# Performance work log

Hardware: AMD Instinct MI355X
Metric: run time of the kernel (lower is better)

Reference implementation:

```python
import jax, jax.numpy as jnp
import numpy as np
import math

ANSWER_LEN = 11; D_MODEL = 6; FFN_DIM = 3; HEAD_DIM = 3; MAX_SEQ_LEN = 34
N_HEADS = 2; POS_DIM = 3; TOK_DIM = 3; VOCAB_SIZE = 14; MAX_DIGITS = 10
EOS_TOKEN = 12; EQUALS_TOKEN = 11; PAD_TOKEN = 13; PLUS_TOKEN = 10
B, T = 65536, 34


def _spiral(i, period):
    return (math.cos(2 * math.pi * i / period), math.sin(2 * math.pi * i / period), i / max(period - 1, 1))


def _build_pos_enc():
    N_POS = 10
    pe = np.zeros((MAX_SEQ_LEN, POS_DIM), dtype=np.float32)
    for i in range(MAX_DIGITS):
        pe[i] = _spiral(i, N_POS)
    for i in range(MAX_DIGITS):
        pe[11 + i] = _spiral(i, N_POS)
    for i in range(min(ANSWER_LEN, N_POS)):
        pe[22 + i] = _spiral(i, N_POS)
    pe[32] = [0.0, 0.0, 1.5]
    pe[10] = [2.0, 0.0, -1.0]
    pe[21] = [0.0, 2.0, -1.0]
    pe[33] = [-2.0, 0.0, -1.0]
    return pe


def _build_tok_emb():
    emb = np.zeros((VOCAB_SIZE, TOK_DIM), dtype=np.float32)
    for d in range(10):
        emb[d] = _spiral(d, 10)
    emb[PLUS_TOKEN] = [2.0, 0.0, -1.0]
    emb[EQUALS_TOKEN] = [0.0, 2.0, -1.0]
    emb[EOS_TOKEN] = [-2.0, 0.0, -1.0]
    emb[PAD_TOKEN] = [0.0, -2.0, -1.0]
    return emb


def setup_inputs() -> dict:
    key = jax.random.key(0)
    ks = jax.random.split(key, 12)
    H = N_HEADS * HEAD_DIM  # 6

    def lin(k, out_d, in_d):
        bound = 1.0 / math.sqrt(in_d)
        return jax.random.uniform(k, (out_d, in_d), jnp.float32, -bound, bound)

    return {
        'idx': jax.random.randint(ks[0], (B, T), 0, VOCAB_SIZE),
        'tok_emb': jnp.asarray(_build_tok_emb()),
        'pos_enc': jnp.asarray(_build_pos_enc()),
        'q_w': lin(ks[1], H, POS_DIM),
        'k_w': lin(ks[2], H, POS_DIM),
        'v_w': lin(ks[3], H, TOK_DIM),
        'out_w': lin(ks[4], D_MODEL, H),
        'ln1_g': jnp.ones((D_MODEL,)), 'ln1_b': jnp.zeros((D_MODEL,)),
        'ln2_g': jnp.ones((D_MODEL,)), 'ln2_b': jnp.zeros((D_MODEL,)),
        'lnf_g': jnp.ones((D_MODEL,)), 'lnf_b': jnp.zeros((D_MODEL,)),
        'ffn_w1': lin(ks[5], FFN_DIM, D_MODEL),
        'ffn_b1': jax.random.uniform(ks[6], (FFN_DIM,), jnp.float32, -1/math.sqrt(D_MODEL), 1/math.sqrt(D_MODEL)),
        'ffn_w2': lin(ks[7], D_MODEL, FFN_DIM),
        'ffn_b2': jax.random.uniform(ks[8], (D_MODEL,), jnp.float32, -1/math.sqrt(FFN_DIM), 1/math.sqrt(FFN_DIM)),
        'head_w': lin(ks[9], TOK_DIM, D_MODEL),
    }


def _ln(x, g, b, eps=1e-5):
    mu = jnp.mean(x, -1, keepdims=True)
    var = jnp.mean((x - mu) ** 2, -1, keepdims=True)
    return (x - mu) * jax.lax.rsqrt(var + eps) * g + b


def reference(idx, tok_emb, pos_enc, q_w, k_w, v_w, out_w,
              ln1_g, ln1_b, ln2_g, ln2_b, lnf_g, lnf_b,
              ffn_w1, ffn_b1, ffn_w2, ffn_b2, head_w):
    b, t = idx.shape
    tok = tok_emb[idx]                              # [B,T,3]
    pos = jnp.broadcast_to(pos_enc[:t][None], (b, t, POS_DIM))
    x = jnp.concatenate([tok, pos], -1)             # [B,T,6]
    h = _ln(x, ln1_g, ln1_b)
    x_tok, x_pos = h[..., :TOK_DIM], h[..., TOK_DIM:]
    q = (x_pos @ q_w.T).reshape(b, t, N_HEADS, HEAD_DIM)
    k = (x_pos @ k_w.T).reshape(b, t, N_HEADS, HEAD_DIM)
    v = (x_tok @ v_w.T).reshape(b, t, N_HEADS, HEAD_DIM)
    attn = jnp.einsum('bqhd,bkhd->bhqk', q, k) / math.sqrt(HEAD_DIM)
    mask = jnp.tril(jnp.ones((t, t), dtype=bool))
    attn = jnp.where(mask[None, None], attn, -jnp.inf)
    attn = jax.nn.softmax(attn, -1)
    out = jnp.einsum('bhqk,bkhd->bqhd', attn, v).reshape(b, t, N_HEADS * HEAD_DIM)
    x = x + out @ out_w.T
    h2 = _ln(x, ln2_g, ln2_b)
    ffn = jax.nn.gelu(h2 @ ffn_w1.T + ffn_b1, approximate=False) @ ffn_w2.T + ffn_b2
    x = x + ffn
    x = _ln(x, lnf_g, lnf_b)
    return (x @ head_w.T) @ tok_emb.T               # [B,T,VOCAB]
```

## Files before the change

### kernel.cpp

```cpp
#include <hip/hip_runtime.h>
#include <math.h>

#define TT  34
#define VV  14
#define BLK 256

#if __has_builtin(__builtin_amdgcn_exp2f)
#define EXP2F(x) __builtin_amdgcn_exp2f(x)
#else
#define EXP2F(x) exp2f(x)
#endif


__global__ __launch_bounds__(BLK) void addtx_fwd(
    const int*   __restrict__ idx,
    const float* __restrict__ tok_emb,
    const float* __restrict__ pos_enc,
    const float* __restrict__ q_w,
    const float* __restrict__ k_w,
    const float* __restrict__ v_w,
    const float* __restrict__ out_w,
    const float* __restrict__ ln1_g, const float* __restrict__ ln1_b,
    const float* __restrict__ ln2_g, const float* __restrict__ ln2_b,
    const float* __restrict__ lnf_g, const float* __restrict__ lnf_b,
    const float* __restrict__ ffn_w1, const float* __restrict__ ffn_b1,
    const float* __restrict__ ffn_w2, const float* __restrict__ ffn_b2,
    const float* __restrict__ head_w,
    float* __restrict__ out)
{
    __shared__ float4 kvs[TT * VV * 3];
    __shared__ float  wsm[336];
    __shared__ int    idsb[308];

    const int tid = threadIdx.x;
    const int blk = blockIdx.x;

    {
        const int i = tid;
        if (i < 36)       wsm[i] = out_w[i];
        else if (i < 42)  wsm[i] = ln2_g[i - 36];
        else if (i < 48)  wsm[i] = ln2_b[i - 42];
        else if (i < 66)  wsm[i] = ffn_w1[i - 48];
        else if (i < 69)  wsm[i] = ffn_b1[i - 66];
        else if (i < 87)  wsm[i] = ffn_w2[i - 69];
        else if (i < 93)  wsm[i] = ffn_b2[i - 87];
        else if (i < 99)  wsm[i] = lnf_g[i - 93];
        else if (i < 105) wsm[i] = lnf_b[i - 99];
        else if (i < 189) {
            const int j = i - 105, v = j / 6, d = j - v * 6;
            wsm[i] = head_w[0 * 6 + d] * tok_emb[v * 3 + 0]
                   + head_w[1 * 6 + d] * tok_emb[v * 3 + 1]
                   + head_w[2 * 6 + d] * tok_emb[v * 3 + 2];
        }
        if (tid < 144) {
            const int k2 = 192 + tid;
            wsm[k2] = (k2 < 234) ? tok_emb[k2 - 192] : pos_enc[k2 - 234];
        }
    }

    const int ntot = (int)gridDim.x * BLK;
    const int b0   = (blk * BLK) / TT;
    {
        const int gb = b0 * TT;
        for (int e = tid; e < 308; e += BLK) {
            const int g = gb + e;
            idsb[e] = (g < ntot) ? idx[g] : 0;
        }
    }

    const float rs3l = 0.57735026918962576f * 1.4426950408889634f;
    for (int e = tid; e < TT * VV; e += BLK) {
        const int pos = e / VV, id = e - pos * VV;
        float x[6];
        x[0] = tok_emb[id * 3 + 0]; x[1] = tok_emb[id * 3 + 1]; x[2] = tok_emb[id * 3 + 2];
        x[3] = pos_enc[pos * 3 + 0]; x[4] = pos_enc[pos * 3 + 1]; x[5] = pos_enc[pos * 3 + 2];
        float mu = (x[0] + x[1] + x[2] + x[3] + x[4] + x[5]) * (1.0f / 6.0f);
        float var = 0.0f;
        #pragma unroll
        for (int d = 0; d < 6; ++d) { float dd = x[d] - mu; var += dd * dd; }
        const float rstd = rsqrtf(var * (1.0f / 6.0f) + 1e-5f);
        float h[6];
        #pragma unroll
        for (int d = 0; d < 6; ++d) h[d] = (x[d] - mu) * rstd * ln1_g[d] + ln1_b[d];
        float kk[6], vvv[6];
        #pragma unroll
        for (int r = 0; r < 6; ++r) {
            kk[r]  = (h[3] * k_w[r * 3 + 0] + h[4] * k_w[r * 3 + 1] + h[5] * k_w[r * 3 + 2]) * rs3l;
            vvv[r] =  h[0] * v_w[r * 3 + 0] + h[1] * v_w[r * 3 + 1] + h[2] * v_w[r * 3 + 2];
        }
        kvs[e * 3 + 0] = make_float4(kk[0], kk[1], kk[2], kk[3]);
        kvs[e * 3 + 1] = make_float4(kk[4], kk[5], vvv[0], vvv[1]);
        kvs[e * 3 + 2] = make_float4(vvv[2], vvv[3], vvv[4], vvv[5]);
    }
    __syncthreads();

    const int srank = (tid + ((blk & 3) << 6)) & (BLK - 1);
    const int r0 = (blk * BLK) % TT;
    const int m  = (TT - r0) % TT;
    int dsel, ksel;
    if (m < 18) {
        const int nA = (18 - m) << 3;
        if (srank < nA)            { dsel = m + (srank >> 3); ksel = srank & 7; }
        else if (srank < nA + 112) { const int r = srank - nA;       dsel = 18 + r / 7; ksel = r % 7; }
        else                       { const int r = srank - nA - 112; dsel = r >> 3;     ksel = r & 7; }
    } else {
        const int nA = (TT - m) * 7;
        if (srank < nA)            { dsel = m + srank / 7; ksel = srank % 7; }
        else if (srank < nA + 144) { const int r = srank - nA;       dsel = r >> 3;     ksel = r & 7; }
        else                       { const int r = srank - nA - 144; dsel = 18 + r / 7; ksel = r % 7; }
    }
    const int il   = dsel + ksel * TT;
    const int flat = blk * BLK + il;
    const int b    = flat / TT;
    const int t    = flat - b * TT;
    const int* __restrict__ rowL = idsb + (b - b0) * TT;

    float x[6];
    {
        const int mid = rowL[t];
        x[0] = wsm[192 + mid * 3]; x[1] = wsm[193 + mid * 3]; x[2] = wsm[194 + mid * 3];
        x[3] = wsm[234 + t * 3];   x[4] = wsm[235 + t * 3];   x[5] = wsm[236 + t * 3];
    }
    float q[6];
    {
        float mu = (x[0] + x[1] + x[2] + x[3] + x[4] + x[5]) * (1.0f / 6.0f);
        float var = 0.0f;
        #pragma unroll
        for (int d = 0; d < 6; ++d) { float dd = x[d] - mu; var += dd * dd; }
        const float rstd = rsqrtf(var * (1.0f / 6.0f) + 1e-5f);
        float h[6];
        #pragma unroll
        for (int d = 0; d < 6; ++d) h[d] = (x[d] - mu) * rstd * ln1_g[d] + ln1_b[d];
        #pragma unroll
        for (int r = 0; r < 6; ++r)
            q[r] = h[3] * q_w[r * 3 + 0] + h[4] * q_w[r * 3 + 1] + h[5] * q_w[r * 3 + 2];
    }

    float l0 = 0.f, l1 = 0.f;
    float a0 = 0.f, a1 = 0.f, a2 = 0.f, a3 = 0.f, a4 = 0.f, a5 = 0.f;
    int ids = rowL[0];
    int sb = 0;
    for (int s = 0; s <= t; ++s) {
        const float4* e4 = kvs + (sb + ids * 3);
        const float4 ka = e4[0];
        const float4 kb = e4[1];
        const float4 vb = e4[2];
        ids = rowL[s + 1];
        const float sc0 = q[0] * ka.x + q[1] * ka.y + q[2] * ka.z;
        const float sc1 = q[3] * ka.w + q[4] * kb.x + q[5] * kb.y;
        const float p0 = EXP2F(sc0);
        const float p1 = EXP2F(sc1);
        l0 += p0; l1 += p1;
        a0 += p0 * kb.z; a1 += p0 * kb.w; a2 += p0 * vb.x;
        a3 += p1 * vb.y; a4 += p1 * vb.z; a5 += p1 * vb.w;
        sb += VV * 3;
    }
    const float i0 = 1.0f / l0, i1 = 1.0f / l1;
    const float o6[6] = { a0 * i0, a1 * i0, a2 * i0, a3 * i1, a4 * i1, a5 * i1 };

    #pragma unroll
    for (int d = 0; d < 6; ++d) {
        float s = x[d];
        #pragma unroll
        for (int j = 0; j < 6; ++j) s += o6[j] * wsm[d * 6 + j];
        x[d] = s;
    }

    {
        float mu = (x[0] + x[1] + x[2] + x[3] + x[4] + x[5]) * (1.0f / 6.0f);
        float var = 0.0f;
        #pragma unroll
        for (int d = 0; d < 6; ++d) { float dd = x[d] - mu; var += dd * dd; }
        const float rstd = rsqrtf(var * (1.0f / 6.0f) + 1e-5f);
        float h2[6];
        #pragma unroll
        for (int d = 0; d < 6; ++d) h2[d] = (x[d] - mu) * rstd * wsm[36 + d] + wsm[42 + d];
        float g3[3];
        #pragma unroll
        for (int i = 0; i < 3; ++i) {
            float f = wsm[66 + i];
            #pragma unroll
            for (int d = 0; d < 6; ++d) f += h2[d] * wsm[48 + i * 6 + d];
            g3[i] = 0.5f * f * (1.0f + erff(f * 0.70710678118654752f));
        }
        #pragma unroll
        for (int d = 0; d < 6; ++d) {
            float s = x[d] + wsm[87 + d];
            #pragma unroll
            for (int i = 0; i < 3; ++i) s += g3[i] * wsm[69 + d * 3 + i];
            x[d] = s;
        }
    }

    float lg[VV];
    {
        float mu = (x[0] + x[1] + x[2] + x[3] + x[4] + x[5]) * (1.0f / 6.0f);
        float var = 0.0f;
        #pragma unroll
        for (int d = 0; d < 6; ++d) { float dd = x[d] - mu; var += dd * dd; }
        const float rstd = rsqrtf(var * (1.0f / 6.0f) + 1e-5f);
        float xf[6];
        #pragma unroll
        for (int d = 0; d < 6; ++d) xf[d] = (x[d] - mu) * rstd * wsm[93 + d] + wsm[99 + d];
        #pragma unroll
        for (int v = 0; v < VV; ++v) {
            float s = 0.0f;
            #pragma unroll
            for (int d = 0; d < 6; ++d) s += xf[d] * wsm[105 + v * 6 + d];
            lg[v] = s;
        }
    }

    __syncthreads();
    float2* lg2 = reinterpret_cast<float2*>(kvs);
    #pragma unroll
    for (int j = 0; j < 7; ++j)
        lg2[il * 7 + j] = make_float2(lg[2 * j], lg[2 * j + 1]);
    __syncthreads();
    const float2* s2 = reinterpret_cast<const float2*>(kvs);
    float2* __restrict__ ob2 = reinterpret_cast<float2*>(out + (size_t)blk * (BLK * VV));
    #pragma unroll
    for (int j = 0; j < 7; ++j)
        ob2[j * BLK + tid] = s2[j * BLK + tid];
}

extern "C" void kernel_launch(void* const* d_in, const int* in_sizes, int n_in,
                              void* d_out, int out_size, void* d_ws, size_t ws_size,
                              hipStream_t stream) {
    const int*   idx     = (const int*)  d_in[0];
    const float* tok_emb = (const float*)d_in[1];
    const float* pos_enc = (const float*)d_in[2];
    const float* q_w     = (const float*)d_in[3];
    const float* k_w     = (const float*)d_in[4];
    const float* v_w     = (const float*)d_in[5];
    const float* out_w   = (const float*)d_in[6];
    const float* ln1_g   = (const float*)d_in[7];
    const float* ln1_b   = (const float*)d_in[8];
    const float* ln2_g   = (const float*)d_in[9];
    const float* ln2_b   = (const float*)d_in[10];
    const float* lnf_g   = (const float*)d_in[11];
    const float* lnf_b   = (const float*)d_in[12];
    const float* ffn_w1  = (const float*)d_in[13];
    const float* ffn_b1  = (const float*)d_in[14];
    const float* ffn_w2  = (const float*)d_in[15];
    const float* ffn_b2  = (const float*)d_in[16];
    const float* head_w  = (const float*)d_in[17];
    float* out = (float*)d_out;

    const int n = in_sizes[0];
    const int blocks = n / BLK;
    addtx_fwd<<<blocks, BLK, 0, stream>>>(idx, tok_emb, pos_enc, q_w, k_w, v_w, out_w,
                                          ln1_g, ln1_b, ln2_g, ln2_b, lnf_g, lnf_b,
                                          ffn_w1, ffn_b1, ffn_w2, ffn_b2, head_w, out);
}
```

Measured before the change: 222.8 us.

## Remap blocks to 64-sequence by 4-position tiles with wave-uniform positions

Each block now handles 64 sequences and a chunk of up to 4 time positions, one wavefront per position. Every lane in a wave therefore runs the same attention loop length, which removes the divergence of the old mixed-position mapping. Block indices are swizzled so the 8 XCDs each take contiguous batch ranges. The idx tile is stored as bytes in a transposed layout, the K/V table is built only for the rows the block needs, and the final layernorm is folded into the head projection. In exchange, each block re-reads the same idx rows across 9 time chunks, and the output writes become strided with partial-row scatter.

```diff
diff --git a/kernel.cpp b/kernel.cpp
--- a/kernel.cpp
+++ b/kernel.cpp
@@ -4,6 +4,9 @@
 #define TT  34
 #define VV  14
 #define BLK 256
+#define BCH 64
+#define NCH 9
+#define IDP 68
 
 #if __has_builtin(__builtin_amdgcn_exp2f)
 #define EXP2F(x) __builtin_amdgcn_exp2f(x)
@@ -29,47 +32,59 @@
     float* __restrict__ out)
 {
     __shared__ float4 kvs[TT * VV * 3];
-    __shared__ float  wsm[336];
-    __shared__ int    idsb[308];
+    __shared__ float  wsm[176];
+    __shared__ unsigned char idsb[35 * IDP];
 
     const int tid = threadIdx.x;
-    const int blk = blockIdx.x;
-
-    {
+
+    const int bx   = blockIdx.x;
+    const int xcd  = bx & 7;
+    const int jj   = bx >> 3;
+    const int jd9  = jj / NCH;
+    const int tc   = jj - jd9 * NCH;
+    const int nbc8 = (int)gridDim.x / (NCH * 8);
+    const int bc   = xcd * nbc8 + jd9;
+    const int b0   = bc * BCH;
+    const int t_base = tc << 2;
+    const int nt   = (tc == 8) ? 2 : 4;
+    const int nst  = t_base + nt + ((tc == 8) ? 0 : 0);
+    const int nrow = (tc == 8) ? TT : (t_base + 4);
+
+    if (tid < 176) {
+        float val = 0.0f;
         const int i = tid;
-        if (i < 36)       wsm[i] = out_w[i];
-        else if (i < 42)  wsm[i] = ln2_g[i - 36];
-        else if (i < 48)  wsm[i] = ln2_b[i - 42];
-        else if (i < 66)  wsm[i] = ffn_w1[i - 48];
-        else if (i < 69)  wsm[i] = ffn_b1[i - 66];
-        else if (i < 87)  wsm[i] = ffn_w2[i - 69];
-        else if (i < 93)  wsm[i] = ffn_b2[i - 87];
-        else if (i < 99)  wsm[i] = lnf_g[i - 93];
-        else if (i < 105) wsm[i] = lnf_b[i - 99];
-        else if (i < 189) {
-            const int j = i - 105, v = j / 6, d = j - v * 6;
-            wsm[i] = head_w[0 * 6 + d] * tok_emb[v * 3 + 0]
-                   + head_w[1 * 6 + d] * tok_emb[v * 3 + 1]
-                   + head_w[2 * 6 + d] * tok_emb[v * 3 + 2];
-        }
-        if (tid < 144) {
-            const int k2 = 192 + tid;
-            wsm[k2] = (k2 < 234) ? tok_emb[k2 - 192] : pos_enc[k2 - 234];
-        }
-    }
-
-    const int ntot = (int)gridDim.x * BLK;
-    const int b0   = (blk * BLK) / TT;
+        if (i < 36)       val = out_w[i];
+        else if (i < 42)  val = ln2_g[i - 36];
+        else if (i < 48)  val = ln2_b[i - 42];
+        else if (i < 66)  val = ffn_w1[i - 48];
+        else if (i < 69)  val = ffn_b1[i - 66];
+        else if (i < 87)  val = ffn_w2[i - 69];
+        else if (i < 93)  val = ffn_b2[i - 87];
+        else if (i < 111) { const int k = i - 93, c = k / 6, d = k - c * 6;
+                            val = lnf_g[d] * head_w[c * 6 + d]; }
+        else if (i < 114) { const int c = i - 111; float s = 0.0f;
+                            #pragma unroll
+                            for (int d = 0; d < 6; ++d) s += lnf_g[d] * head_w[c * 6 + d];
+                            val = s; }
+        else if (i < 117) { const int c = i - 114; float s = 0.0f;
+                            #pragma unroll
+                            for (int d = 0; d < 6; ++d) s += lnf_b[d] * head_w[c * 6 + d];
+                            val = s; }
+        else if (i >= 120 && i < 162) val = tok_emb[i - 120];
+        wsm[i] = val;
+    }
+
     {
         const int gb = b0 * TT;
-        for (int e = tid; e < 308; e += BLK) {
-            const int g = gb + e;
-            idsb[e] = (g < ntot) ? idx[g] : 0;
-        }
+        for (int e = tid; e < BCH * TT; e += BLK) {
+            const int bl = e / TT, s = e - bl * TT;
+            idsb[s * IDP + bl] = (unsigned char)idx[gb + e];
+        }
+        if (tid < BCH) idsb[TT * IDP + tid] = 0;
     }
 
     const float rs3l = 0.57735026918962576f * 1.4426950408889634f;
-    for (int e = tid; e < TT * VV; e += BLK) {
+    for (int e = tid; e < nrow * VV; e += BLK) {
         const int pos = e / VV, id = e - pos * VV;
         float x[6];
         x[0] = tok_emb[id * 3 + 0]; x[1] = tok_emb[id * 3 + 1]; x[2] = tok_emb[id * 3 + 2];
@@ -94,134 +109,129 @@
     }
     __syncthreads();
 
-    const int srank = (tid + ((blk & 3) << 6)) & (BLK - 1);
-    const int r0 = (blk * BLK) % TT;
-    const int m  = (TT - r0) % TT;
-    int dsel, ksel;
-    if (m < 18) {
-        const int nA = (18 - m) << 3;
-        if (srank < nA)            { dsel = m + (srank >> 3); ksel = srank & 7; }
-        else if (srank < nA + 112) { const int r = srank - nA;       dsel = 18 + r / 7; ksel = r % 7; }
-        else                       { const int r = srank - nA - 112; dsel = r >> 3;     ksel = r & 7; }
-    } else {
-        const int nA = (TT - m) * 7;
-        if (srank < nA)            { dsel = m + srank / 7; ksel = srank % 7; }
-        else if (srank < nA + 144) { const int r = srank - nA;       dsel = r >> 3;     ksel = r & 7; }
-        else                       { const int r = srank - nA - 144; dsel = 18 + r / 7; ksel = r % 7; }
-    }
-    const int il   = dsel + ksel * TT;
-    const int flat = blk * BLK + il;
-    const int b    = flat / TT;
-    const int t    = flat - b * TT;
-    const int* __restrict__ rowL = idsb + (b - b0) * TT;
-
-    float x[6];
-    {
-        const int mid = rowL[t];
-        x[0] = wsm[192 + mid * 3]; x[1] = wsm[193 + mid * 3]; x[2] = wsm[194 + mid * 3];
-        x[3] = wsm[234 + t * 3];   x[4] = wsm[235 + t * 3];   x[5] = wsm[236 + t * 3];
-    }
-    float q[6];
-    {
-        float mu = (x[0] + x[1] + x[2] + x[3] + x[4] + x[5]) * (1.0f / 6.0f);
-        float var = 0.0f;
-        #pragma unroll
-        for (int d = 0; d < 6; ++d) { float dd = x[d] - mu; var += dd * dd; }
-        const float rstd = rsqrtf(var * (1.0f / 6.0f) + 1e-5f);
-        float h[6];
-        #pragma unroll
-        for (int d = 0; d < 6; ++d) h[d] = (x[d] - mu) * rstd * ln1_g[d] + ln1_b[d];
-        #pragma unroll
-        for (int r = 0; r < 6; ++r)
-            q[r] = h[3] * q_w[r * 3 + 0] + h[4] * q_w[r * 3 + 1] + h[5] * q_w[r * 3 + 2];
-    }
-
-    float l0 = 0.f, l1 = 0.f;
-    float a0 = 0.f, a1 = 0.f, a2 = 0.f, a3 = 0.f, a4 = 0.f, a5 = 0.f;
-    int ids = rowL[0];
-    int sb = 0;
-    for (int s = 0; s <= t; ++s) {
-        const float4* e4 = kvs + (sb + ids * 3);
-        const float4 ka = e4[0];
-        const float4 kb = e4[1];
-        const float4 vb = e4[2];
-        ids = rowL[s + 1];
-        const float sc0 = q[0] * ka.x + q[1] * ka.y + q[2] * ka.z;
-        const float sc1 = q[3] * ka.w + q[4] * kb.x + q[5] * kb.y;
-        const float p0 = EXP2F(sc0);
-        const float p1 = EXP2F(sc1);
-        l0 += p0; l1 += p1;
-        a0 += p0 * kb.z; a1 += p0 * kb.w; a2 += p0 * vb.x;
-        a3 += p1 * vb.y; a4 += p1 * vb.z; a5 += p1 * vb.w;
-        sb += VV * 3;
-    }
-    const float i0 = 1.0f / l0, i1 = 1.0f / l1;
-    const float o6[6] = { a0 * i0, a1 * i0, a2 * i0, a3 * i1, a4 * i1, a5 * i1 };
-
-    #pragma unroll
-    for (int d = 0; d < 6; ++d) {
-        float s = x[d];
-        #pragma unroll
-        for (int j = 0; j < 6; ++j) s += o6[j] * wsm[d * 6 + j];
-        x[d] = s;
-    }
-
-    {
-        float mu = (x[0] + x[1] + x[2] + x[3] + x[4] + x[5]) * (1.0f / 6.0f);
-        float var = 0.0f;
-        #pragma unroll
-        for (int d = 0; d < 6; ++d) { float dd = x[d] - mu; var += dd * dd; }
-        const float rstd = rsqrtf(var * (1.0f / 6.0f) + 1e-5f);
-        float h2[6];
-        #pragma unroll
-        for (int d = 0; d < 6; ++d) h2[d] = (x[d] - mu) * rstd * wsm[36 + d] + wsm[42 + d];
-        float g3[3];
-        #pragma unroll
-        for (int i = 0; i < 3; ++i) {
-            float f = wsm[66 + i];
-            #pragma unroll
-            for (int d = 0; d < 6; ++d) f += h2[d] * wsm[48 + i * 6 + d];
-            g3[i] = 0.5f * f * (1.0f + erff(f * 0.70710678118654752f));
-        }
+    const int w = tid >> 6, lane = tid & 63;
+    const int t = t_base + w;
+    const bool active = (t < TT);
+    float lg[VV];
+
+    if (active) {
+        const int myid = (int)idsb[t * IDP + lane];
+        float x[6];
+        x[0] = wsm[120 + myid * 3]; x[1] = wsm[121 + myid * 3]; x[2] = wsm[122 + myid * 3];
+        x[3] = pos_enc[t * 3 + 0];  x[4] = pos_enc[t * 3 + 1];  x[5] = pos_enc[t * 3 + 2];
+
+        float q[6];
+        {
+            float mu = (x[0] + x[1] + x[2] + x[3] + x[4] + x[5]) * (1.0f / 6.0f);
+            float var = 0.0f;
+            #pragma unroll
+            for (int d = 0; d < 6; ++d) { float dd = x[d] - mu; var += dd * dd; }
+            const float rstd = rsqrtf(var * (1.0f / 6.0f) + 1e-5f);
+            const float h3 = (x[3] - mu) * rstd * ln1_g[3] + ln1_b[3];
+            const float h4 = (x[4] - mu) * rstd * ln1_g[4] + ln1_b[4];
+            const float h5 = (x[5] - mu) * rstd * ln1_g[5] + ln1_b[5];
+            #pragma unroll
+            for (int r = 0; r < 6; ++r)
+                q[r] = h3 * q_w[r * 3 + 0] + h4 * q_w[r * 3 + 1] + h5 * q_w[r * 3 + 2];
+        }
+
+        float l0 = 0.f, l1 = 0.f;
+        float a0 = 0.f, a1 = 0.f, a2 = 0.f, a3 = 0.f, a4 = 0.f, a5 = 0.f;
+        const unsigned char* ip = idsb + lane;
+        int ids = (int)ip[0];
+        const float4* kp = kvs;
+        for (int s = 0; s <= t; ++s) {
+            const float4* e4 = kp + ids * 3;
+            const float4 ka = e4[0];
+            const float4 kb = e4[1];
+            const float4 vb = e4[2];
+            ids = (int)ip[(s + 1) * IDP];
+            const float sc0 = q[0] * ka.x + q[1] * ka.y + q[2] * ka.z;
+            const float sc1 = q[3] * ka.w + q[4] * kb.x + q[5] * kb.y;
+            const float p0 = EXP2F(sc0);
+            const float p1 = EXP2F(sc1);
+            l0 += p0; l1 += p1;
+            a0 += p0 * kb.z; a1 += p0 * kb.w; a2 += p0 * vb.x;
+            a3 += p1 * vb.y; a4 += p1 * vb.z; a5 += p1 * vb.w;
+            kp += VV * 3;
+        }
+        const float i0 = 1.0f / l0, i1 = 1.0f / l1;
+        const float o6[6] = { a0 * i0, a1 * i0, a2 * i0, a3 * i1, a4 * i1, a5 * i1 };
+
         #pragma unroll
         for (int d = 0; d < 6; ++d) {
-            float s = x[d] + wsm[87 + d];
-            #pragma unroll
-            for (int i = 0; i < 3; ++i) s += g3[i] * wsm[69 + d * 3 + i];
+            float s = x[d];
+            #pragma unroll
+            for (int j = 0; j < 6; ++j) s += o6[j] * wsm[d * 6 + j];
             x[d] = s;
         }
-    }
-
-    float lg[VV];
-    {
-        float mu = (x[0] + x[1] + x[2] + x[3] + x[4] + x[5]) * (1.0f / 6.0f);
-        float var = 0.0f;
-        #pragma unroll
-        for (int d = 0; d < 6; ++d) { float dd = x[d] - mu; var += dd * dd; }
-        const float rstd = rsqrtf(var * (1.0f / 6.0f) + 1e-5f);
-        float xf[6];
-        #pragma unroll
-        for (int d = 0; d < 6; ++d) xf[d] = (x[d] - mu) * rstd * wsm[93 + d] + wsm[99 + d];
-        #pragma unroll
-        for (int v = 0; v < VV; ++v) {
-            float s = 0.0f;
-            #pragma unroll
-            for (int d = 0; d < 6; ++d) s += xf[d] * wsm[105 + v * 6 + d];
-            lg[v] = s;
-        }
-    }
-
+
+        {
+            float mu = (x[0] + x[1] + x[2] + x[3] + x[4] + x[5]) * (1.0f / 6.0f);
+            float var = 0.0f;
+            #pragma unroll
+            for (int d = 0; d < 6; ++d) { float dd = x[d] - mu; var += dd * dd; }
+            const float rstd = rsqrtf(var * (1.0f / 6.0f) + 1e-5f);
+            float h2[6];
+            #pragma unroll
+            for (int d = 0; d < 6; ++d) h2[d] = (x[d] - mu) * rstd * wsm[36 + d] + wsm[42 + d];
+            float g3[3];
+            #pragma unroll
+            for (int i = 0; i < 3; ++i) {
+                float f = wsm[66 + i];
+                #pragma unroll
+                for (int d = 0; d < 6; ++d) f += h2[d] * wsm[48 + i * 6 + d];
+                g3[i] = 0.5f * f * (1.0f + erff(f * 0.70710678118654752f));
+            }
+            #pragma unroll
+            for (int d = 0; d < 6; ++d) {
+                float s = x[d] + wsm[87 + d];
+                #pragma unroll
+                for (int i = 0; i < 3; ++i) s += g3[i] * wsm[69 + d * 3 + i];
+                x[d] = s;
+            }
+        }
+
+        {
+            float mu = (x[0] + x[1] + x[2] + x[3] + x[4] + x[5]) * (1.0f / 6.0f);
+            float var = 0.0f;
+            #pragma unroll
+            for (int d = 0; d < 6; ++d) { float dd = x[d] - mu; var += dd * dd; }
+            const float rstd = rsqrtf(var * (1.0f / 6.0f) + 1e-5f);
+            float y[3];
+            #pragma unroll
+            for (int c = 0; c < 3; ++c) {
+                float dot = 0.0f;
+                #pragma unroll
+                for (int d = 0; d < 6; ++d) dot += x[d] * wsm[93 + c * 6 + d];
+                y[c] = rstd * (dot - mu * wsm[111 + c]) + wsm[114 + c];
+            }
+            #pragma unroll
+            for (int v = 0; v < VV; ++v)
+                lg[v] = y[0] * wsm[120 + v * 3] + y[1] * wsm[121 + v * 3] + y[2] * wsm[122 + v * 3];
+        }
+    }
     __syncthreads();
-    float2* lg2 = reinterpret_cast<float2*>(kvs);
-    #pragma unroll
-    for (int j = 0; j < 7; ++j)
-        lg2[il * 7 + j] = make_float2(lg[2 * j], lg[2 * j + 1]);
+
+    float* lgs = reinterpret_cast<float*>(kvs);
+    if (active) {
+        #pragma unroll
+        for (int p = 0; p < 7; ++p)
+            *reinterpret_cast<float2*>(&lgs[lane * 58 + w * 14 + 2 * p]) =
+                make_float2(lg[2 * p], lg[2 * p + 1]);
+    }
     __syncthreads();
-    const float2* s2 = reinterpret_cast<const float2*>(kvs);
-    float2* __restrict__ ob2 = reinterpret_cast<float2*>(out + (size_t)blk * (BLK * VV));
-    #pragma unroll
-    for (int j = 0; j < 7; ++j)
-        ob2[j * BLK + tid] = s2[j * BLK + tid];
+
+    const int n7 = nt * BCH * 7;
+    const int sh = (tc == 8) ? 1 : 2;
+    float* __restrict__ obase = out + (size_t)b0 * (TT * VV) + t_base * VV;
+    for (int f = tid; f < n7; f += BLK) {
+        const int q7 = f / 7, r7 = f - q7 * 7;
+        const int bl2 = q7 >> sh, wsel = q7 & (nt - 1);
+        const float2 v2 = *reinterpret_cast<const float2*>(&lgs[bl2 * 58 + wsel * 14 + 2 * r7]);
+        *reinterpret_cast<float2*>(&obase[bl2 * (TT * VV) + wsel * VV + 2 * r7]) = v2;
+    }
+    (void)nst;
 }
 
 extern "C" void kernel_launch(void* const* d_in, const int* in_sizes, int n_in,
@@ -247,8 +257,9 @@
     const float* head_w  = (const float*)d_in[17];
     float* out = (float*)d_out;
 
-    const int n = in_sizes[0];
-    const int blocks = n / BLK;
+    const int n  = in_sizes[0];
+    const int nb = n / TT;
+    const int blocks = (nb / BCH) * NCH;
     addtx_fwd<<<blocks, BLK, 0, stream>>>(idx, tok_emb, pos_enc, q_w, k_w, v_w, out_w,
                                           ln1_g, ln1_b, ln2_g, ln2_b, lnf_g, lnf_b,
                                           ffn_w1, ffn_b1, ffn_w2, ffn_b2, head_w, out);
```

Result: slower. 246.3 us (+10.6%).

## Vectorize per-token math with packed float2 FMAs and fold LN-final into the head

Applied to the files above, without the earlier changes.

Rewrites the attention accumulation, out-projection, FFN and final head with two-wide packed FMA vectors, reordering the K/V shared layout and the weight tables so pairs load as float2. The final LayerNorm gain and bias are folded into head_w, so logits come from a three-dimensional projection times tok_emb, which cuts the per-token multiply count. Token ids are pre-scaled to byte offsets so the attention loop drops an index multiply, and an approximate reciprocal replaces the divide. The goal is to lower VALU instruction count on the mi355x packed-math path, at the cost of slightly different rounding.

```diff
diff --git a/kernel.cpp b/kernel.cpp
--- a/kernel.cpp
+++ b/kernel.cpp
@@ -4,12 +4,26 @@
 #define TT  34
 #define VV  14
 #define BLK 256
+
+typedef float v2f __attribute__((ext_vector_type(2)));
+typedef float v4f __attribute__((ext_vector_type(4)));
 
 #if __has_builtin(__builtin_amdgcn_exp2f)
 #define EXP2F(x) __builtin_amdgcn_exp2f(x)
 #else
 #define EXP2F(x) exp2f(x)
 #endif
+#if __has_builtin(__builtin_amdgcn_rcpf)
+#define RCPF(x) __builtin_amdgcn_rcpf(x)
+#else
+#define RCPF(x) (1.0f/(x))
+#endif
+
+static __device__ __forceinline__ v2f fma2(v2f a, v2f b, v2f c) {
+    return __builtin_elementwise_fma(a, b, c);
+}
+static __device__ __forceinline__ v2f bc2(float s) { v2f r; r.x = s; r.y = s; return r; }
+#define SV2(v, a, b) __builtin_shufflevector((v), (v), (a), (b))
 
 
 __global__ __launch_bounds__(BLK) void addtx_fwd(
@@ -28,34 +42,37 @@
     const float* __restrict__ head_w,
     float* __restrict__ out)
 {
-    __shared__ float4 kvs[TT * VV * 3];
-    __shared__ float  wsm[336];
-    __shared__ int    idsb[308];
+    __shared__ v4f   kvs[TT * VV * 3];
+    __shared__ float wsm[308];
+    __shared__ int   idsb[308];
 
     const int tid = threadIdx.x;
     const int blk = blockIdx.x;
 
-    {
-        const int i = tid;
-        if (i < 36)       wsm[i] = out_w[i];
-        else if (i < 42)  wsm[i] = ln2_g[i - 36];
-        else if (i < 48)  wsm[i] = ln2_b[i - 42];
-        else if (i < 66)  wsm[i] = ffn_w1[i - 48];
-        else if (i < 69)  wsm[i] = ffn_b1[i - 66];
-        else if (i < 87)  wsm[i] = ffn_w2[i - 69];
-        else if (i < 93)  wsm[i] = ffn_b2[i - 87];
-        else if (i < 99)  wsm[i] = lnf_g[i - 93];
-        else if (i < 105) wsm[i] = lnf_b[i - 99];
-        else if (i < 189) {
-            const int j = i - 105, v = j / 6, d = j - v * 6;
-            wsm[i] = head_w[0 * 6 + d] * tok_emb[v * 3 + 0]
-                   + head_w[1 * 6 + d] * tok_emb[v * 3 + 1]
-                   + head_w[2 * 6 + d] * tok_emb[v * 3 + 2];
-        }
-        if (tid < 144) {
-            const int k2 = 192 + tid;
-            wsm[k2] = (k2 < 234) ? tok_emb[k2 - 192] : pos_enc[k2 - 234];
-        }
+    for (int i = tid; i < 308; i += BLK) {
+        float val = 0.0f;
+        if (i < 36)       { const int j = i / 6, d = i - j * 6; val = out_w[d * 6 + j]; }
+        else if (i < 42)  val = ln2_g[i - 36];
+        else if (i < 48)  val = ln2_b[i - 42];
+        else if (i < 60)  { const int k = i - 48, d = k >> 1, ii = k & 1; val = ffn_w1[ii * 6 + d]; }
+        else if (i < 66)  val = ffn_w1[12 + (i - 60)];
+        else if (i < 69)  val = ffn_b1[i - 66];
+        else if (i < 70)  val = 0.0f;
+        else if (i < 88)  { const int k = i - 70, ii = k / 6, d = k - ii * 6; val = ffn_w2[d * 3 + ii]; }
+        else if (i < 94)  val = ffn_b2[i - 88];
+        else if (i < 96)  val = 0.0f;
+        else if (i < 108) { const int k = i - 96, d = k >> 1, c = k & 1; val = lnf_g[d] * head_w[c * 6 + d]; }
+        else if (i < 114) { const int d = i - 108; val = lnf_g[d] * head_w[12 + d]; }
+        else if (i < 118) val = 0.0f;
+        else if (i < 121) { const int c = i - 118; float s = 0.0f;
+                            #pragma unroll
+                            for (int d = 0; d < 6; ++d) s += lnf_b[d] * head_w[c * 6 + d];
+                            val = s; }
+        else if (i < 122) val = 0.0f;
+        else if (i < 164) { const int k = i - 122, c = k / 14, v = k - c * 14; val = tok_emb[v * 3 + c]; }
+        else if (i < 206) val = tok_emb[i - 164];
+        else              val = pos_enc[i - 206];
+        wsm[i] = val;
     }
 
     const int ntot = (int)gridDim.x * BLK;
@@ -64,7 +81,7 @@
         const int gb = b0 * TT;
         for (int e = tid; e < 308; e += BLK) {
             const int g = gb + e;
-            idsb[e] = (g < ntot) ? idx[g] : 0;
+            idsb[e] = (g < ntot) ? (idx[g] * 48) : 0;
         }
     }
 
@@ -88,9 +105,12 @@
             kk[r]  = (h[3] * k_w[r * 3 + 0] + h[4] * k_w[r * 3 + 1] + h[5] * k_w[r * 3 + 2]) * rs3l;
             vvv[r] =  h[0] * v_w[r * 3 + 0] + h[1] * v_w[r * 3 + 1] + h[2] * v_w[r * 3 + 2];
         }
-        kvs[e * 3 + 0] = make_float4(kk[0], kk[1], kk[2], kk[3]);
-        kvs[e * 3 + 1] = make_float4(kk[4], kk[5], vvv[0], vvv[1]);
-        kvs[e * 3 + 2] = make_float4(vvv[2], vvv[3], vvv[4], vvv[5]);
+        v4f f0; f0.x = kk[0]; f0.y = kk[3]; f0.z = kk[1]; f0.w = kk[4];
+        v4f f1; f1.x = kk[2]; f1.y = kk[5]; f1.z = vvv[0]; f1.w = vvv[3];
+        v4f f2; f2.x = vvv[1]; f2.y = vvv[4]; f2.z = vvv[2]; f2.w = vvv[5];
+        kvs[e * 3 + 0] = f0;
+        kvs[e * 3 + 1] = f1;
+        kvs[e * 3 + 2] = f2;
     }
     __syncthreads();
 
@@ -117,9 +137,9 @@
 
     float x[6];
     {
-        const int mid = rowL[t];
-        x[0] = wsm[192 + mid * 3]; x[1] = wsm[193 + mid * 3]; x[2] = wsm[194 + mid * 3];
-        x[3] = wsm[234 + t * 3];   x[4] = wsm[235 + t * 3];   x[5] = wsm[236 + t * 3];
+        const int tb = rowL[t] >> 4;
+        x[0] = wsm[164 + tb]; x[1] = wsm[165 + tb]; x[2] = wsm[166 + tb];
+        x[3] = wsm[206 + t * 3]; x[4] = wsm[207 + t * 3]; x[5] = wsm[208 + t * 3];
     }
     float q[6];
     {
@@ -128,97 +148,113 @@
         #pragma unroll
         for (int d = 0; d < 6; ++d) { float dd = x[d] - mu; var += dd * dd; }
         const float rstd = rsqrtf(var * (1.0f / 6.0f) + 1e-5f);
-        float h[6];
-        #pragma unroll
-        for (int d = 0; d < 6; ++d) h[d] = (x[d] - mu) * rstd * ln1_g[d] + ln1_b[d];
+        const float h3 = (x[3] - mu) * rstd * ln1_g[3] + ln1_b[3];
+        const float h4 = (x[4] - mu) * rstd * ln1_g[4] + ln1_b[4];
+        const float h5 = (x[5] - mu) * rstd * ln1_g[5] + ln1_b[5];
         #pragma unroll
         for (int r = 0; r < 6; ++r)
-            q[r] = h[3] * q_w[r * 3 + 0] + h[4] * q_w[r * 3 + 1] + h[5] * q_w[r * 3 + 2];
-    }
-
-    float l0 = 0.f, l1 = 0.f;
-    float a0 = 0.f, a1 = 0.f, a2 = 0.f, a3 = 0.f, a4 = 0.f, a5 = 0.f;
-    int ids = rowL[0];
-    int sb = 0;
+            q[r] = h3 * q_w[r * 3 + 0] + h4 * q_w[r * 3 + 1] + h5 * q_w[r * 3 + 2];
+    }
+    const v2f Q03 = {q[0], q[3]}, Q14 = {q[1], q[4]}, Q25 = {q[2], q[5]};
+
+    v2f L = {0.f, 0.f}, A0 = {0.f, 0.f}, A1 = {0.f, 0.f}, A2 = {0.f, 0.f};
+    int ids48 = rowL[0];
+    const char* kp = (const char*)kvs;
     for (int s = 0; s <= t; ++s) {
-        const float4* e4 = kvs + (sb + ids * 3);
-        const float4 ka = e4[0];
-        const float4 kb = e4[1];
-        const float4 vb = e4[2];
-        ids = rowL[s + 1];
-        const float sc0 = q[0] * ka.x + q[1] * ka.y + q[2] * ka.z;
-        const float sc1 = q[3] * ka.w + q[4] * kb.x + q[5] * kb.y;
-        const float p0 = EXP2F(sc0);
-        const float p1 = EXP2F(sc1);
-        l0 += p0; l1 += p1;
-        a0 += p0 * kb.z; a1 += p0 * kb.w; a2 += p0 * vb.x;
-        a3 += p1 * vb.y; a4 += p1 * vb.z; a5 += p1 * vb.w;
-        sb += VV * 3;
-    }
-    const float i0 = 1.0f / l0, i1 = 1.0f / l1;
-    const float o6[6] = { a0 * i0, a1 * i0, a2 * i0, a3 * i1, a4 * i1, a5 * i1 };
-
+        const v4f* e4 = (const v4f*)(kp + ids48);
+        const v4f ka = e4[0], kb = e4[1], vb = e4[2];
+        ids48 = rowL[s + 1];
+        v2f sc = fma2(Q03, SV2(ka, 0, 1),
+                 fma2(Q14, SV2(ka, 2, 3),
+                      Q25 * SV2(kb, 0, 1)));
+        v2f p; p.x = EXP2F(sc.x); p.y = EXP2F(sc.y);
+        L += p;
+        A0 = fma2(p, SV2(kb, 2, 3), A0);
+        A1 = fma2(p, SV2(vb, 0, 1), A1);
+        A2 = fma2(p, SV2(vb, 2, 3), A2);
+        kp += VV * 48;
+    }
+    v2f I; I.x = RCPF(L.x); I.y = RCPF(L.y);
+    const v2f O0 = A0 * I, O1 = A1 * I, O2 = A2 * I;
+    const float o6[6] = {O0.x, O1.x, O2.x, O0.y, O1.y, O2.y};
+
+    v2f X0 = {x[0], x[1]}, X1 = {x[2], x[3]}, X2 = {x[4], x[5]};
+    #define LD2(i) (*reinterpret_cast<const v2f*>(&wsm[(i)]))
     #pragma unroll
-    for (int d = 0; d < 6; ++d) {
-        float s = x[d];
-        #pragma unroll
-        for (int j = 0; j < 6; ++j) s += o6[j] * wsm[d * 6 + j];
-        x[d] = s;
-    }
-
-    {
-        float mu = (x[0] + x[1] + x[2] + x[3] + x[4] + x[5]) * (1.0f / 6.0f);
-        float var = 0.0f;
-        #pragma unroll
-        for (int d = 0; d < 6; ++d) { float dd = x[d] - mu; var += dd * dd; }
-        const float rstd = rsqrtf(var * (1.0f / 6.0f) + 1e-5f);
-        float h2[6];
-        #pragma unroll
-        for (int d = 0; d < 6; ++d) h2[d] = (x[d] - mu) * rstd * wsm[36 + d] + wsm[42 + d];
+    for (int j = 0; j < 6; ++j) {
+        const v2f oj = bc2(o6[j]);
+        X0 = fma2(oj, LD2(j * 6 + 0), X0);
+        X1 = fma2(oj, LD2(j * 6 + 2), X1);
+        X2 = fma2(oj, LD2(j * 6 + 4), X2);
+    }
+
+    {
+        v2f S = X0 + X1 + X2;
+        const float mu = (S.x + S.y) * (1.0f / 6.0f);
+        const v2f muv = bc2(mu);
+        const v2f D0 = X0 - muv, D1 = X1 - muv, D2 = X2 - muv;
+        v2f E = fma2(D0, D0, fma2(D1, D1, D2 * D2));
+        const float rstd = rsqrtf((E.x + E.y) * (1.0f / 6.0f) + 1e-5f);
+        const v2f rs = bc2(rstd);
+        const v2f H0 = fma2(D0 * rs, LD2(36), LD2(42));
+        const v2f H1 = fma2(D1 * rs, LD2(38), LD2(44));
+        const v2f H2 = fma2(D2 * rs, LD2(40), LD2(46));
+        const float h[6] = {H0.x, H0.y, H1.x, H1.y, H2.x, H2.y};
+        v2f F = LD2(66);
+        float f2 = wsm[68];
+        #pragma unroll
+        for (int d = 0; d < 6; ++d) {
+            F  = fma2(bc2(h[d]), LD2(48 + 2 * d), F);
+            f2 = fmaf(h[d], wsm[60 + d], f2);
+        }
         float g3[3];
+        g3[0] = 0.5f * F.x * (1.0f + erff(F.x * 0.70710678118654752f));
+        g3[1] = 0.5f * F.y * (1.0f + erff(F.y * 0.70710678118654752f));
+        g3[2] = 0.5f * f2  * (1.0f + erff(f2  * 0.70710678118654752f));
+        X0 += LD2(88); X1 += LD2(90); X2 += LD2(92);
         #pragma unroll
         for (int i = 0; i < 3; ++i) {
-            float f = wsm[66 + i];
-            #pragma unroll
-            for (int d = 0; d < 6; ++d) f += h2[d] * wsm[48 + i * 6 + d];
-            g3[i] = 0.5f * f * (1.0f + erff(f * 0.70710678118654752f));
-        }
+            const v2f gi = bc2(g3[i]);
+            X0 = fma2(gi, LD2(70 + i * 6 + 0), X0);
+            X1 = fma2(gi, LD2(70 + i * 6 + 2), X1);
+            X2 = fma2(gi, LD2(70 + i * 6 + 4), X2);
+        }
+    }
+
+    v2f lgv[7];
+    {
+        v2f S = X0 + X1 + X2;
+        const float mu = (S.x + S.y) * (1.0f / 6.0f);
+        const v2f muv = bc2(mu);
+        const v2f D0 = X0 - muv, D1 = X1 - muv, D2 = X2 - muv;
+        v2f E = fma2(D0, D0, fma2(D1, D1, D2 * D2));
+        const float rstd = rsqrtf((E.x + E.y) * (1.0f / 6.0f) + 1e-5f);
+        const float xd[6] = {D0.x, D0.y, D1.x, D1.y, D2.x, D2.y};
+        v2f D01 = {0.f, 0.f};
+        float d2 = 0.f;
         #pragma unroll
         for (int d = 0; d < 6; ++d) {
-            float s = x[d] + wsm[87 + d];
-            #pragma unroll
-            for (int i = 0; i < 3; ++i) s += g3[i] * wsm[69 + d * 3 + i];
-            x[d] = s;
-        }
-    }
-
-    float lg[VV];
-    {
-        float mu = (x[0] + x[1] + x[2] + x[3] + x[4] + x[5]) * (1.0f / 6.0f);
-        float var = 0.0f;
-        #pragma unroll
-        for (int d = 0; d < 6; ++d) { float dd = x[d] - mu; var += dd * dd; }
-        const float rstd = rsqrtf(var * (1.0f / 6.0f) + 1e-5f);
-        float xf[6];
-        #pragma unroll
-        for (int d = 0; d < 6; ++d) xf[d] = (x[d] - mu) * rstd * wsm[93 + d] + wsm[99 + d];
-        #pragma unroll
-        for (int v = 0; v < VV; ++v) {
-            float s = 0.0f;
-            #pragma unroll
-            for (int d = 0; d < 6; ++d) s += xf[d] * wsm[105 + v * 6 + d];
-            lg[v] = s;
-        }
-    }
-
+            D01 = fma2(bc2(xd[d]), LD2(96 + 2 * d), D01);
+            d2  = fmaf(xd[d], wsm[108 + d], d2);
+        }
+        const v2f y01 = fma2(bc2(rstd), D01, LD2(118));
+        const float y2 = fmaf(rstd, d2, wsm[120]);
+        const v2f Y0 = bc2(y01.x), Y1 = bc2(y01.y), Y2 = bc2(y2);
+        #pragma unroll
+        for (int mm = 0; mm < 7; ++mm)
+            lgv[mm] = fma2(Y0, LD2(122 + 2 * mm),
+                      fma2(Y1, LD2(136 + 2 * mm),
+                           Y2 * LD2(150 + 2 * mm)));
+    }
     __syncthreads();
-    float2* lg2 = reinterpret_cast<float2*>(kvs);
+
+    v2f* lg2 = reinterpret_cast<v2f*>(kvs);
     #pragma unroll
     for (int j = 0; j < 7; ++j)
-        lg2[il * 7 + j] = make_float2(lg[2 * j], lg[2 * j + 1]);
+        lg2[il * 7 + j] = lgv[j];
     __syncthreads();
-    const float2* s2 = reinterpret_cast<const float2*>(kvs);
-    float2* __restrict__ ob2 = reinterpret_cast<float2*>(out + (size_t)blk * (BLK * VV));
+    const v2f* s2 = reinterpret_cast<const v2f*>(kvs);
+    v2f* __restrict__ ob2 = reinterpret_cast<v2f*>(out + (size_t)blk * (BLK * VV));
     #pragma unroll
     for (int j = 0; j < 7; ++j)
         ob2[j * BLK + tid] = s2[j * BLK + tid];
```

New measurement: 213.3 us. 4.2% less time.
